# Optimization experiments

Measured on AMD Instinct MI355X. Metric: run time of the kernel, lower is better.

## Reference

```python
import jax, jax.numpy as jnp
import numpy as np

HIDDEN = 1024
NUM_HEADS = 16
HEAD_DIM = 64
B, S = 2, 2048


def setup_inputs() -> dict:
    key = jax.random.key(0)
    k1, k2, k3 = jax.random.split(key, 3)
    x = jax.random.normal(k1, (B, S, HIDDEN), dtype=jnp.float32)
    # xavier-uniform style scaling for the projection weights
    lim_qkv = (6.0 / (HIDDEN + 3 * NUM_HEADS * HEAD_DIM)) ** 0.5
    lim_o = (6.0 / (NUM_HEADS * HEAD_DIM + HIDDEN)) ** 0.5
    w_qkv = jax.random.uniform(k2, (HIDDEN, 3 * NUM_HEADS * HEAD_DIM), jnp.float32, -lim_qkv, lim_qkv)
    w_o = jax.random.uniform(k3, (NUM_HEADS * HEAD_DIM, HIDDEN), jnp.float32, -lim_o, lim_o)
    return {"x": x, "w_qkv": w_qkv, "w_o": w_o}


def reference(x, w_qkv, w_o):
    b, s, _ = x.shape
    qkv = jnp.einsum('bsh,hf->bsf', x, w_qkv)               # [b, s, 3*H*D]
    qkv = qkv.reshape(b, s, 3, NUM_HEADS, HEAD_DIM)
    q = jnp.transpose(qkv[:, :, 0], (0, 2, 1, 3))           # [b, h, s, d]
    k = jnp.transpose(qkv[:, :, 1], (0, 2, 3, 1))           # [b, h, d, s]
    v = jnp.transpose(qkv[:, :, 2], (0, 2, 1, 3))           # [b, h, s, d]
    scores = jnp.einsum('bhqd,bhdk->bhqk', q, k) / jnp.sqrt(jnp.float32(HEAD_DIM))
    scores = jax.nn.softmax(scores, axis=-1)                # [b, h, q, k]
    # NOTE: faithful to source bug: sums over q, output indexed by k
    values = jnp.einsum('bhqk,bhkd->bhkd', scores, v)       # [b, h, s, d]
    values = jnp.transpose(values, (0, 2, 1, 3)).reshape(b, s, NUM_HEADS * HEAD_DIM)
    return jnp.einsum('bsf,fh->bsh', values, w_o)
```

## Files before the change

kernel.cpp:

```cpp
#include <hip/hip_runtime.h>
#include <stdint.h>


#define DEV static __device__ __forceinline__

typedef unsigned short u16;
typedef __attribute__((ext_vector_type(4))) float f32x4;
typedef __attribute__((ext_vector_type(16))) float f32x16;
typedef __bf16 bf16x8 __attribute__((ext_vector_type(8)));
typedef __attribute__((ext_vector_type(8))) unsigned short u16x8;
typedef __attribute__((ext_vector_type(4))) unsigned short u16x4;

#define QSCALE 0.18033688011112042f

DEV u16 f2bf(float f) {
    unsigned u = __builtin_bit_cast(unsigned, f);
    u += 0x7fffu + ((u >> 16) & 1u);
    return (u16)(u >> 16);
}
DEV float bf2f(u16 h) {
    unsigned u = ((unsigned)h) << 16;
    return __builtin_bit_cast(float, u);
}

DEV void async_copy16(const void* g, void* l) {
    __builtin_amdgcn_global_load_lds(
        (__attribute__((address_space(1))) void*)(g),
        (__attribute__((address_space(3))) void*)(l), 16, 0, 0);
}

__global__ __launch_bounds__(256) void prep(
    const float* __restrict__ x, u16* __restrict__ xb,
    const float* __restrict__ wqkv, u16* __restrict__ wqkvT,
    const float* __restrict__ wo, u16* __restrict__ woT) {
    __shared__ float tile[32][33];
    const int bid = blockIdx.x;
    const int t = threadIdx.x;
    if (bid < 4096) {
        int i = bid * 256 + t;
        f32x4 v = *(const f32x4*)(x + (size_t)i * 4);
        u16x4 o;
#pragma unroll
        for (int j = 0; j < 4; j++) o[j] = f2bf(v[j]);
        *(u16x4*)(xb + (size_t)i * 4) = o;
        return;
    }
    const float* src;
    u16* dst;
    int rows, cols, c0, r0;
    if (bid < 7168) {
        int b2 = bid - 4096;
        src = wqkv; dst = wqkvT; rows = 1024; cols = 3072;
        c0 = (b2 % 96) * 32; r0 = (b2 / 96) * 32;
    } else {
        int b3 = bid - 7168;
        src = wo; dst = woT; rows = 1024; cols = 1024;
        c0 = (b3 % 32) * 32; r0 = (b3 / 32) * 32;
    }
    int tx = t & 31, ty = t >> 5;
#pragma unroll
    for (int i = 0; i < 4; i++)
        tile[ty + i * 8][tx] = src[(size_t)(r0 + ty + i * 8) * cols + c0 + tx];
    __syncthreads();
#pragma unroll
    for (int i = 0; i < 4; i++)
        dst[(size_t)(c0 + ty + i * 8) * rows + r0 + tx] = f2bf(tile[tx][ty + i * 8]);
}

__global__ __launch_bounds__(256) void gemm_qkv(
    const u16* __restrict__ A, const u16* __restrict__ Bt,
    u16* __restrict__ qb, u16* __restrict__ kb, u16* __restrict__ vb) {
    __shared__ __align__(16) u16 smem[128 * 136];
    u16* As = smem;
    u16* Bs = smem + 4096;
    const int t = threadIdx.x;
    const int wave = t >> 6;
    const int lane = t & 63;
    const int quad = lane >> 4;
    const int l16 = lane & 15;
    const int wr = wave >> 1;
    const int wc = wave & 1;
    const int m0 = blockIdx.y * 128;
    const int n0 = blockIdx.x * 128;

    f32x4 acc[4][4];
#pragma unroll
    for (int i = 0; i < 4; i++)
#pragma unroll
        for (int j = 0; j < 4; j++) acc[i][j] = {0.f, 0.f, 0.f, 0.f};

    for (int kt = 0; kt < 1024; kt += 32) {
#pragma unroll
        for (int i = 0; i < 2; i++) {
            int idx = i * 256 + t;
            int row = idx >> 2, kc = idx & 3;
            async_copy16(A + (size_t)(m0 + row) * 1024 + kt + kc * 8, &As[idx * 8]);
            async_copy16(Bt + (size_t)(n0 + row) * 1024 + kt + kc * 8, &Bs[idx * 8]);
        }
        __syncthreads();
        bf16x8 af[4], bfr[4];
#pragma unroll
        for (int mt = 0; mt < 4; mt++)
            af[mt] = *(const bf16x8*)&As[(wr * 64 + mt * 16 + l16) * 32 + quad * 8];
#pragma unroll
        for (int nt = 0; nt < 4; nt++)
            bfr[nt] = *(const bf16x8*)&Bs[(wc * 64 + nt * 16 + l16) * 32 + quad * 8];
#pragma unroll
        for (int mt = 0; mt < 4; mt++)
#pragma unroll
            for (int nt = 0; nt < 4; nt++)
                acc[mt][nt] = __builtin_amdgcn_mfma_f32_16x16x32_bf16(
                    af[mt], bfr[nt], acc[mt][nt], 0, 0, 0);
        __syncthreads();
    }

    const int tsel = n0 >> 10;
    u16* dst = tsel == 0 ? qb : (tsel == 1 ? kb : vb);
    const float scl = tsel == 0 ? QSCALE : 1.0f;
#pragma unroll
    for (int mt = 0; mt < 4; mt++)
#pragma unroll
        for (int nt = 0; nt < 4; nt++) {
            int nn = wc * 64 + nt * 16 + l16;
#pragma unroll
            for (int r = 0; r < 4; r++) {
                int mm = wr * 64 + mt * 16 + quad * 4 + r;
                smem[mm * 136 + nn] = f2bf(acc[mt][nt][r] * scl);
            }
        }
    __syncthreads();
    const int col0 = (l16) * 8;
    const int rowb = (t >> 4);
    const int h0 = (n0 & 1023) >> 6;
#pragma unroll
    for (int i = 0; i < 8; i++) {
        int row = i * 16 + rowb;
        u16x8 v = *(const u16x8*)&smem[row * 136 + col0];
        int h = h0 + (col0 >> 6), d = col0 & 63;
        int mm = m0 + row;
        int b = mm >> 11, s = mm & 2047;
        *(u16x8*)&dst[((size_t)((b * 16 + h) * 2048 + s)) * 64 + d] = v;
    }
}

__global__ __launch_bounds__(256) void gemm_out(
    const u16* __restrict__ vb, const float* __restrict__ csum,
    const u16* __restrict__ Bt, float* __restrict__ out) {
    __shared__ __align__(16) u16 As[64 * 32];
    __shared__ __align__(16) u16 Bs[128 * 32];
    const int m0 = blockIdx.y * 64;
    const int n0 = blockIdx.x * 128;
    const int t = threadIdx.x;
    const int wave = t >> 6, lane = t & 63;
    const int quad = lane >> 4, l16 = lane & 15;
    const int wr = wave >> 1, wc = wave & 1;

    const int arow = m0 + (t >> 2);
    const int ab = arow >> 11, as = arow & 2047;

    f32x4 acc[2][4];
#pragma unroll
    for (int i = 0; i < 2; i++)
#pragma unroll
        for (int j = 0; j < 4; j++) acc[i][j] = {0.f, 0.f, 0.f, 0.f};

    for (int kt = 0; kt < 1024; kt += 32) {
        {
            int c = kt + (t & 3) * 8;
            int h = c >> 6, d0 = c & 63;
            int bh = ab * 16 + h;
            float cs = csum[bh * 2048 + as];
            u16x8 v = *(const u16x8*)&vb[((size_t)(bh * 2048 + as)) * 64 + d0];
            u16x8 o;
#pragma unroll
            for (int i = 0; i < 8; i++) o[i] = f2bf(bf2f(v[i]) * cs);
            *(u16x8*)&As[t * 8] = o;
        }
#pragma unroll
        for (int i = 0; i < 2; i++) {
            int idx = i * 256 + t;
            int row = idx >> 2, kc = idx & 3;
            async_copy16(Bt + (size_t)(n0 + row) * 1024 + kt + kc * 8, &Bs[idx * 8]);
        }
        __syncthreads();
        bf16x8 af[2], bfr[4];
#pragma unroll
        for (int mt = 0; mt < 2; mt++)
            af[mt] = *(const bf16x8*)&As[(wr * 32 + mt * 16 + l16) * 32 + quad * 8];
#pragma unroll
        for (int nt = 0; nt < 4; nt++)
            bfr[nt] = *(const bf16x8*)&Bs[(wc * 64 + nt * 16 + l16) * 32 + quad * 8];
#pragma unroll
        for (int mt = 0; mt < 2; mt++)
#pragma unroll
            for (int nt = 0; nt < 4; nt++)
                acc[mt][nt] = __builtin_amdgcn_mfma_f32_16x16x32_bf16(
                    af[mt], bfr[nt], acc[mt][nt], 0, 0, 0);
        __syncthreads();
    }
#pragma unroll
    for (int nt = 0; nt < 4; nt++) {
        int nn = n0 + wc * 64 + nt * 16 + l16;
#pragma unroll
        for (int mt = 0; mt < 2; mt++) {
#pragma unroll
            for (int r = 0; r < 4; r++) {
                int mm = m0 + wr * 32 + mt * 16 + quad * 4 + r;
                out[(size_t)mm * 1024 + nn] = acc[mt][nt][r];
            }
        }
    }
}


#define WAITBAR_4 asm volatile("s_waitcnt vmcnt(4)\n\ts_barrier" ::: "memory")
#define WAITBAR_0 asm volatile("s_waitcnt vmcnt(0)\n\ts_barrier" ::: "memory")
#define BAR_ONLY  asm volatile("s_barrier" ::: "memory")

__global__ __launch_bounds__(256) void attn_pass1(
    const u16* __restrict__ qb, const u16* __restrict__ kb,
    float* __restrict__ lp) {
    __shared__ __align__(16) u16 Ks[2][128 * 64];
    const int t = threadIdx.x;
    const int wave = t >> 6;
    const int lane = t & 63;
    const int l32 = lane & 31, half = lane >> 5;
    const int kchunk = blockIdx.x & 3;
    const int qblk = (blockIdx.x >> 2) & 7;
    const int bh = blockIdx.x >> 5;
    const int q0 = qblk * 256 + wave * 64;

    bf16x8 a[2][4];
#pragma unroll
    for (int qs = 0; qs < 2; qs++) {
        const u16* Qr = qb + (size_t)(bh * 2048 + q0 + qs * 32 + l32) * 64 + half * 8;
#pragma unroll
        for (int f = 0; f < 4; f++) a[qs][f] = *(const bf16x8*)&Qr[f * 16];
    }

    const u16* Kbase = kb + (size_t)(bh * 2048 + kchunk * 512) * 64;

    float lsum[2][16];
#pragma unroll
    for (int qs = 0; qs < 2; qs++)
#pragma unroll
        for (int r = 0; r < 16; r++) lsum[qs][r] = 0.f;

    f32x16 ZZ;
#pragma unroll
    for (int r = 0; r < 16; r++) ZZ[r] = 0.f;

#define STAGE_K(buf, kt)                                                        \
    {                                                                           \
        _Pragma("unroll") for (int i = 0; i < 4; i++) {                         \
            int idx = i * 256 + t;                                              \
            int row = idx >> 3;                                                 \
            int blk = (idx & 7) ^ (row & 7);                                    \
            async_copy16(Kbase + (size_t)((kt) * 128 + row) * 64 + blk * 8,     \
                         &Ks[buf][idx * 8]);                                    \
        }                                                                       \
    }

#define COMPUTE_K(cur)                                                          \
    {                                                                           \
        _Pragma("unroll") for (int sub = 0; sub < 4; sub++) {                   \
            const int row = sub * 32 + l32;                                     \
            const int r7 = row & 7;                                             \
            bf16x8 bfr[4];                                                      \
            _Pragma("unroll") for (int f = 0; f < 4; f++)                       \
                bfr[f] = *(const bf16x8*)&Ks[cur][row * 64 +                    \
                                                 (((f * 2 + half)) ^ r7) * 8];  \
            __builtin_amdgcn_s_setprio(1);                                      \
            _Pragma("unroll") for (int qs = 0; qs < 2; qs++) {                  \
                f32x16 acc = __builtin_amdgcn_mfma_f32_32x32x16_bf16(           \
                    a[qs][0], bfr[0], ZZ, 0, 0, 0);                             \
                _Pragma("unroll") for (int f = 1; f < 4; f++)                   \
                    acc = __builtin_amdgcn_mfma_f32_32x32x16_bf16(              \
                        a[qs][f], bfr[f], acc, 0, 0, 0);                        \
                __builtin_amdgcn_s_setprio(0);                                  \
                _Pragma("unroll") for (int r = 0; r < 16; r++)                  \
                    lsum[qs][r] += __builtin_amdgcn_exp2f(acc[r]);              \
                __builtin_amdgcn_s_setprio(1);                                  \
            }                                                                   \
            __builtin_amdgcn_s_setprio(0);                                     \
        }                                                                       \
    }

    STAGE_K(0, 0);
    for (int kt = 0; kt < 3; kt++) {
        const int cur = kt & 1;
        STAGE_K(cur ^ 1, kt + 1);
        WAITBAR_4;
        COMPUTE_K(cur);
        BAR_ONLY;
    }
    WAITBAR_0;
    COMPUTE_K(1);

#pragma unroll
    for (int qs = 0; qs < 2; qs++) {
#pragma unroll
        for (int r = 0; r < 16; r++) {
            float v = lsum[qs][r];
            v += __shfl_xor(v, 1);
            v += __shfl_xor(v, 2);
            v += __shfl_xor(v, 4);
            v += __shfl_xor(v, 8);
            v += __shfl_xor(v, 16);
            lsum[qs][r] = v;
        }
    }
    if (l32 == 0) {
#pragma unroll
        for (int qs = 0; qs < 2; qs++) {
            float* dst = lp + kchunk * 65536 + bh * 2048 + q0 + qs * 32 + half * 4;
#pragma unroll
            for (int r = 0; r < 16; r++)
                dst[(r & 3) + 8 * (r >> 2)] = lsum[qs][r];
        }
    }
}

__global__ __launch_bounds__(256) void attn_pass2(
    const u16* __restrict__ qb, const u16* __restrict__ kb,
    const float* __restrict__ lp, float* __restrict__ csum) {
    __shared__ __align__(16) u16 Qs[2][128 * 64];
    __shared__ __align__(16) float li_lds[512];
    const int t = threadIdx.x;
    const int wave = t >> 6;
    const int lane = t & 63;
    const int l32 = lane & 31, half = lane >> 5;
    const int qchunk = blockIdx.x & 3;
    const int kblk = (blockIdx.x >> 2) & 7;
    const int bh = blockIdx.x >> 5;
    const int k0 = kblk * 256 + wave * 64;

    {
        const int base = bh * 2048 + qchunk * 512;
#pragma unroll
        for (int i = 0; i < 2; i++) {
            int q = i * 256 + t;
            float s = lp[base + q] + lp[65536 + base + q] + lp[131072 + base + q] +
                      lp[196608 + base + q];
            li_lds[q] = 1.0f / s;
        }
    }

    bf16x8 b[2][4];
#pragma unroll
    for (int ks = 0; ks < 2; ks++) {
        const u16* Kr = kb + (size_t)(bh * 2048 + k0 + ks * 32 + l32) * 64 + half * 8;
#pragma unroll
        for (int f = 0; f < 4; f++) b[ks][f] = *(const bf16x8*)&Kr[f * 16];
    }

    const u16* Qbase = qb + (size_t)(bh * 2048 + qchunk * 512) * 64;

    f32x16 ZZ;
#pragma unroll
    for (int r = 0; r < 16; r++) ZZ[r] = 0.f;

#define STAGE_Q(buf, qt)                                                        \
    {                                                                           \
        _Pragma("unroll") for (int i = 0; i < 4; i++) {                         \
            int idx = i * 256 + t;                                              \
            int row = idx >> 3;                                                 \
            int blk = (idx & 7) ^ (row & 7);                                    \
            async_copy16(Qbase + (size_t)((qt) * 128 + row) * 64 + blk * 8,     \
                         &Qs[buf][idx * 8]);                                    \
        }                                                                       \
    }

#define COMPUTE_Q(cur, qt)                                                      \
    {                                                                           \
        _Pragma("unroll") for (int sub = 0; sub < 4; sub++) {                   \
            const int row = sub * 32 + l32;                                     \
            const int r7 = row & 7;                                             \
            bf16x8 af[4];                                                       \
            _Pragma("unroll") for (int f = 0; f < 4; f++)                       \
                af[f] = *(const bf16x8*)&Qs[cur][row * 64 +                     \
                                                 (((f * 2 + half)) ^ r7) * 8];  \
            const float* lr = &li_lds[(qt) * 128 + sub * 32 + half * 4];        \
            f32x4 li0 = *(const f32x4*)&lr[0];                                  \
            f32x4 li1 = *(const f32x4*)&lr[8];                                  \
            f32x4 li2 = *(const f32x4*)&lr[16];                                 \
            f32x4 li3 = *(const f32x4*)&lr[24];                                 \
            __builtin_amdgcn_s_setprio(1);                                      \
            _Pragma("unroll") for (int ks = 0; ks < 2; ks++) {                  \
                f32x16 acc = __builtin_amdgcn_mfma_f32_32x32x16_bf16(           \
                    af[0], b[ks][0], ZZ, 0, 0, 0);                              \
                _Pragma("unroll") for (int f = 1; f < 4; f++)                   \
                    acc = __builtin_amdgcn_mfma_f32_32x32x16_bf16(              \
                        af[f], b[ks][f], acc, 0, 0, 0);                         \
                __builtin_amdgcn_s_setprio(0);                                  \
                float c = cs[ks];                                               \
                _Pragma("unroll") for (int r = 0; r < 4; r++)                   \
                    c += __builtin_amdgcn_exp2f(acc[r]) * li0[r];               \
                _Pragma("unroll") for (int r = 0; r < 4; r++)                   \
                    c += __builtin_amdgcn_exp2f(acc[4 + r]) * li1[r];           \
                _Pragma("unroll") for (int r = 0; r < 4; r++)                   \
                    c += __builtin_amdgcn_exp2f(acc[8 + r]) * li2[r];           \
                _Pragma("unroll") for (int r = 0; r < 4; r++)                   \
                    c += __builtin_amdgcn_exp2f(acc[12 + r]) * li3[r];          \
                cs[ks] = c;                                                     \
                __builtin_amdgcn_s_setprio(1);                                  \
            }                                                                   \
            __builtin_amdgcn_s_setprio(0);                                     \
        }                                                                       \
    }

    float cs[2] = {0.f, 0.f};
    __syncthreads();
    STAGE_Q(0, 0);

    for (int qt = 0; qt < 3; qt++) {
        const int cur = qt & 1;
        STAGE_Q(cur ^ 1, qt + 1);
        WAITBAR_4;
        COMPUTE_Q(cur, qt);
        BAR_ONLY;
    }
    WAITBAR_0;
    COMPUTE_Q(1, 3);

#pragma unroll
    for (int ks = 0; ks < 2; ks++) {
        float v = cs[ks] + __shfl_xor(cs[ks], 32);
        if (lane < 32)
            atomicAdd(&csum[bh * 2048 + k0 + ks * 32 + lane], v);
    }
}


extern "C" void kernel_launch(void* const* d_in, const int* in_sizes, int n_in,
                              void* d_out, int out_size, void* d_ws, size_t ws_size,
                              hipStream_t stream) {
    const float* x    = (const float*)d_in[0];
    const float* wqkv = (const float*)d_in[1];
    const float* wo   = (const float*)d_in[2];
    float* out = (float*)d_out;
    char* ws = (char*)d_ws;

    u16* xb      = (u16*)(ws);
    u16* wqkvT   = (u16*)(ws + 8388608);
    u16* woT     = (u16*)(ws + 14680064);
    u16* qb      = (u16*)(ws + 16777216);
    u16* kb      = (u16*)(ws + 25165824);
    u16* vb      = (u16*)(ws + 33554432);
    float* lp    = (float*)(ws);
    float* csum  = (float*)(ws + 1048576);

    prep<<<8192, 256, 0, stream>>>(x, xb, wqkv, wqkvT, wo, woT);
    gemm_qkv<<<dim3(24, 32), 256, 0, stream>>>(xb, wqkvT, qb, kb, vb);
    hipMemsetAsync(csum, 0, 262144, stream);
    attn_pass1<<<1024, 256, 0, stream>>>(qb, kb, lp);
    attn_pass2<<<1024, 256, 0, stream>>>(qb, kb, lp, csum);
    gemm_out<<<dim3(8, 64), 256, 0, stream>>>(vb, csum, woT, out);
}
```

Before: 202.5 us.

## Double-buffer QKV GEMM loads, swizzle block order, fold csum zeroing into pass1

The QKV projection GEMM now issues the async global-to-LDS copies for the next K tile before computing on the current one, using two LDS buffers and explicit vmcnt waits so load latency overlaps MFMA work. Blocks launch on a 1D grid remapped by a swizzle, which changes the order in which output tiles are scheduled and may improve L2 reuse. The separate memset of the column-sum buffer is removed. Instead, the first 256 blocks of attn_pass1 zero it, and the buffer moves to a non-aliased workspace offset so it no longer overlaps xb/lp. This saves one launch but relies on pass1 finishing before pass2 accumulates into csum.

```diff
diff --git a/kernel.cpp b/kernel.cpp
--- a/kernel.cpp
+++ b/kernel.cpp
@@ -28,6 +28,10 @@
         (__attribute__((address_space(1))) void*)(g),
         (__attribute__((address_space(3))) void*)(l), 16, 0, 0);
 }
+
+#define WAITBAR_4 asm volatile("s_waitcnt vmcnt(4)\n\ts_barrier" ::: "memory")
+#define WAITBAR_0 asm volatile("s_waitcnt vmcnt(0)\n\ts_barrier" ::: "memory")
+#define BAR_ONLY  asm volatile("s_barrier" ::: "memory")
 
 __global__ __launch_bounds__(256) void prep(
     const float* __restrict__ x, u16* __restrict__ xb,
@@ -71,8 +75,6 @@
     const u16* __restrict__ A, const u16* __restrict__ Bt,
     u16* __restrict__ qb, u16* __restrict__ kb, u16* __restrict__ vb) {
     __shared__ __align__(16) u16 smem[128 * 136];
-    u16* As = smem;
-    u16* Bs = smem + 4096;
     const int t = threadIdx.x;
     const int wave = t >> 6;
     const int lane = t & 63;
@@ -80,8 +82,10 @@
     const int l16 = lane & 15;
     const int wr = wave >> 1;
     const int wc = wave & 1;
-    const int m0 = blockIdx.y * 128;
-    const int n0 = blockIdx.x * 128;
+    const int bid = blockIdx.x;
+    const int swz = (bid & 7) * 96 + (bid >> 3);
+    const int n0 = (swz % 24) * 128;
+    const int m0 = (swz / 24) * 128;
 
     f32x4 acc[4][4];
 #pragma unroll
@@ -89,30 +93,46 @@
 #pragma unroll
         for (int j = 0; j < 4; j++) acc[i][j] = {0.f, 0.f, 0.f, 0.f};
 
-    for (int kt = 0; kt < 1024; kt += 32) {
-#pragma unroll
-        for (int i = 0; i < 2; i++) {
-            int idx = i * 256 + t;
-            int row = idx >> 2, kc = idx & 3;
-            async_copy16(A + (size_t)(m0 + row) * 1024 + kt + kc * 8, &As[idx * 8]);
-            async_copy16(Bt + (size_t)(n0 + row) * 1024 + kt + kc * 8, &Bs[idx * 8]);
-        }
-        __syncthreads();
-        bf16x8 af[4], bfr[4];
-#pragma unroll
-        for (int mt = 0; mt < 4; mt++)
-            af[mt] = *(const bf16x8*)&As[(wr * 64 + mt * 16 + l16) * 32 + quad * 8];
-#pragma unroll
-        for (int nt = 0; nt < 4; nt++)
-            bfr[nt] = *(const bf16x8*)&Bs[(wc * 64 + nt * 16 + l16) * 32 + quad * 8];
-#pragma unroll
-        for (int mt = 0; mt < 4; mt++)
-#pragma unroll
-            for (int nt = 0; nt < 4; nt++)
-                acc[mt][nt] = __builtin_amdgcn_mfma_f32_16x16x32_bf16(
-                    af[mt], bfr[nt], acc[mt][nt], 0, 0, 0);
-        __syncthreads();
-    }
+#define QKV_STAGE(buf, col)                                                     \
+    {                                                                           \
+        _Pragma("unroll") for (int i = 0; i < 2; i++) {                         \
+            int idx = i * 256 + t;                                              \
+            int row = idx >> 2, kc = idx & 3;                                   \
+            async_copy16(A + (size_t)(m0 + row) * 1024 + (col) + kc * 8,        \
+                         &smem[(buf) * 8192 + idx * 8]);                        \
+            async_copy16(Bt + (size_t)(n0 + row) * 1024 + (col) + kc * 8,       \
+                         &smem[(buf) * 8192 + 4096 + idx * 8]);                 \
+        }                                                                       \
+    }
+
+#define QKV_COMPUTE(buf)                                                        \
+    {                                                                           \
+        bf16x8 af[4], bfr[4];                                                   \
+        _Pragma("unroll") for (int mt = 0; mt < 4; mt++)                        \
+            af[mt] = *(const bf16x8*)&smem[(buf) * 8192 +                       \
+                                           (wr * 64 + mt * 16 + l16) * 32 +    \
+                                           quad * 8];                           \
+        _Pragma("unroll") for (int nt = 0; nt < 4; nt++)                        \
+            bfr[nt] = *(const bf16x8*)&smem[(buf) * 8192 + 4096 +               \
+                                            (wc * 64 + nt * 16 + l16) * 32 +   \
+                                            quad * 8];                          \
+        _Pragma("unroll") for (int mt = 0; mt < 4; mt++)                        \
+            _Pragma("unroll") for (int nt = 0; nt < 4; nt++)                    \
+                acc[mt][nt] = __builtin_amdgcn_mfma_f32_16x16x32_bf16(          \
+                    af[mt], bfr[nt], acc[mt][nt], 0, 0, 0);                     \
+    }
+
+    QKV_STAGE(0, 0);
+    for (int ks = 0; ks < 31; ks++) {
+        const int cur = ks & 1;
+        QKV_STAGE(cur ^ 1, (ks + 1) * 32);
+        WAITBAR_4;
+        QKV_COMPUTE(cur);
+        BAR_ONLY;
+    }
+    WAITBAR_0;
+    QKV_COMPUTE(1);
+    BAR_ONLY;
 
     const int tsel = n0 >> 10;
     u16* dst = tsel == 0 ? qb : (tsel == 1 ? kb : vb);
@@ -213,13 +233,9 @@
 }
 
 
-#define WAITBAR_4 asm volatile("s_waitcnt vmcnt(4)\n\ts_barrier" ::: "memory")
-#define WAITBAR_0 asm volatile("s_waitcnt vmcnt(0)\n\ts_barrier" ::: "memory")
-#define BAR_ONLY  asm volatile("s_barrier" ::: "memory")
-
 __global__ __launch_bounds__(256) void attn_pass1(
     const u16* __restrict__ qb, const u16* __restrict__ kb,
-    float* __restrict__ lp) {
+    float* __restrict__ lp, float* __restrict__ csum) {
     __shared__ __align__(16) u16 Ks[2][128 * 64];
     const int t = threadIdx.x;
     const int wave = t >> 6;
@@ -229,6 +245,8 @@
     const int qblk = (blockIdx.x >> 2) & 7;
     const int bh = blockIdx.x >> 5;
     const int q0 = qblk * 256 + wave * 64;
+
+    if (blockIdx.x < 256) csum[blockIdx.x * 256 + t] = 0.f;
 
     bf16x8 a[2][4];
 #pragma unroll
@@ -448,12 +466,11 @@
     u16* kb      = (u16*)(ws + 25165824);
     u16* vb      = (u16*)(ws + 33554432);
     float* lp    = (float*)(ws);
-    float* csum  = (float*)(ws + 1048576);
+    float* csum  = (float*)(ws + 42467328);
 
     prep<<<8192, 256, 0, stream>>>(x, xb, wqkv, wqkvT, wo, woT);
-    gemm_qkv<<<dim3(24, 32), 256, 0, stream>>>(xb, wqkvT, qb, kb, vb);
-    hipMemsetAsync(csum, 0, 262144, stream);
-    attn_pass1<<<1024, 256, 0, stream>>>(qb, kb, lp);
+    gemm_qkv<<<768, 256, 0, stream>>>(xb, wqkvT, qb, kb, vb);
+    attn_pass1<<<1024, 256, 0, stream>>>(qb, kb, lp, csum);
     attn_pass2<<<1024, 256, 0, stream>>>(qb, kb, lp, csum);
     gemm_out<<<dim3(8, 64), 256, 0, stream>>>(vb, csum, woT, out);
 }
```

Result: no change. 199.7 us (-1.4%).
